# Kernel tuning notes

Measured on AMD Instinct MI355X. Metric: run time of the kernel, lower is better.

Reference implementation:

```python
import jax, jax.numpy as jnp
import numpy as np

SEQ_LEN = 1024
BATCH = 1024
TAG = 32
START = TAG - 2  # '[CLS]'
END = TAG - 1    # '[SEP]'
NEG = -10000.0


def setup_inputs() -> dict:
    key = jax.random.key(0)
    k1, k2, k3 = jax.random.split(key, 3)
    feats = jax.random.normal(k1, (SEQ_LEN, BATCH, TAG), dtype=jnp.float32)
    # valid-length mask: 1.0 for t < length, else 0.0 (float, as torch multiplies by it)
    lengths = jax.random.randint(k2, (BATCH,), SEQ_LEN // 2, SEQ_LEN + 1)
    mask = (jnp.arange(SEQ_LEN)[:, None] < lengths[None, :]).astype(jnp.float32)
    # transition parameter with forbidden moves into START and out of END
    transition = jax.random.normal(k3, (TAG, TAG), dtype=jnp.float32)
    transition = transition.at[START, :].set(NEG).at[:, END].set(NEG)
    return {"feats": feats, "mask": mask, "transition": transition}


def reference(feats, mask, transition):
    # feats: (S, B, T), mask: (S, B), transition: (T, T)
    batch, tag = feats.shape[1], feats.shape[2]
    alpha0 = jnp.full((batch, tag), NEG, dtype=feats.dtype).at[:, START].set(0.0)

    def step(alpha, xs):
        feat_t, mask_t = xs  # (B, T), (B,)
        # score[b, next, prev] = alpha[b, prev] + transition[next, prev] + feat_t[b, next]
        score = alpha[:, None, :] + transition[None, :, :] + feat_t[:, :, None]
        new_alpha = jax.nn.logsumexp(score, axis=-1)  # (B, T)
        m = mask_t[:, None]
        return new_alpha * m + alpha * (1.0 - m), None

    alpha, _ = jax.lax.scan(step, alpha0, (feats, mask))
    alpha = alpha + transition[END][None, :]
    return jax.nn.logsumexp(alpha, axis=-1)  # (B,)
```

## Files before the change

kernel.cpp:

```cpp
#include <hip/hip_runtime.h>

#define SEQ   1024
#define BATCH 1024
#define TAG   32
#define START 30
#define ENDT  31
#define PFD   8
#define HALF  512

__device__ __forceinline__ float rdlane(float v, int j) {
    return __uint_as_float(__builtin_amdgcn_readlane(__float_as_uint(v), j));
}

__device__ __forceinline__ void gather_dot(float v, const float* __restrict__ coef,
                                           float post, float& vn, float& lg) {
    float r[32];
    #pragma unroll
    for (int j = 0; j < 32; ++j) r[j] = rdlane(v, j);
    __builtin_amdgcn_sched_barrier(0);

    float s0 = r[0] * coef[0];
    float s1 = r[1] * coef[1];
    float s2 = r[2] * coef[2];
    float s3 = r[3] * coef[3];
    float s4 = r[4] * coef[4];
    float s5 = r[5] * coef[5];
    float s6 = r[6] * coef[6];
    float s7 = r[7] * coef[7];
    #pragma unroll
    for (int j = 1; j < 4; ++j) {
        s0 = fmaf(r[8 * j + 0], coef[8 * j + 0], s0);
        s1 = fmaf(r[8 * j + 1], coef[8 * j + 1], s1);
        s2 = fmaf(r[8 * j + 2], coef[8 * j + 2], s2);
        s3 = fmaf(r[8 * j + 3], coef[8 * j + 3], s3);
        s4 = fmaf(r[8 * j + 4], coef[8 * j + 4], s4);
        s5 = fmaf(r[8 * j + 5], coef[8 * j + 5], s5);
        s6 = fmaf(r[8 * j + 6], coef[8 * j + 6], s6);
        s7 = fmaf(r[8 * j + 7], coef[8 * j + 7], s7);
    }
    float dot = ((s0 + s1) + (s2 + s3)) + ((s4 + s5) + (s6 + s7));

    float c  = fmaxf(r[0], 1e-20f);
    float rr = __builtin_amdgcn_rcpf(c);
    lg = __logf(c);
    float sc = post * rr;
    vn = dot * sc;
}

__device__ __forceinline__ void crf_core(float v, float fval,
                                         const float* __restrict__ e,
                                         float& vn, float& lg) {
    gather_dot(v, e, __expf(fval), vn, lg);
}

__device__ void slow_path(const float* __restrict__ feats,
                          const float* __restrict__ mask,
                          const float* __restrict__ trans,
                          float* __restrict__ out, int b, int lane) {
    const int i = lane & 31;
    float e[32];
    {
        const float4* tr4 = reinterpret_cast<const float4*>(trans + i * TAG);
        #pragma unroll
        for (int c = 0; c < 8; ++c) {
            float4 t = tr4[c];
            e[4 * c + 0] = __expf(t.x);
            e[4 * c + 1] = __expf(t.y);
            e[4 * c + 2] = __expf(t.z);
            e[4 * c + 3] = __expf(t.w);
        }
    }
    const float* fp = feats + (unsigned)(b * TAG + i);
    const float* mk = mask + (unsigned)b;

    float  v  = (i == START) ? 1.0f : 0.0f;
    double mA = 0.0;

    float fb[PFD], mb[PFD];
    #pragma unroll
    for (int p = 0; p < PFD; ++p) {
        fb[p] = fp[(unsigned)p << 15];
        mb[p] = mk[(unsigned)p << 10];
    }
    for (int t = 0; t < SEQ; t += PFD) {
        #pragma unroll
        for (int p = 0; p < PFD; ++p) {
            unsigned mu = __builtin_amdgcn_readfirstlane(__float_as_uint(mb[p]));
            float fv = fb[p];
            int tn = t + PFD + p; tn = (tn < SEQ) ? tn : (SEQ - 1);
            fb[p] = fp[(unsigned)tn << 15];
            mb[p] = mk[(unsigned)tn << 10];
            if (mu != 0u) {
                float vn, lg;
                crf_core(v, fv, e, vn, lg);
                if (mu == 0x3f800000u) {
                    v = vn;
                    mA += (double)lg;
                } else {
                    float m   = __uint_as_float(mu);
                    float lv  = __logf(fmaxf(v,  1e-37f));
                    float lvn = __logf(fmaxf(vn, 1e-37f));
                    v = v * __expf(m * (lvn - lv));
                    mA += (double)(m * lg);
                }
            }
        }
    }
    float z = v * __expf(trans[ENDT * TAG + i]);
    float mx = z;
    #pragma unroll
    for (int k = 16; k >= 1; k >>= 1)
        mx = fmaxf(mx, __shfl_xor(mx, k, 32));
    float ss = z * __builtin_amdgcn_rcpf(mx);
    #pragma unroll
    for (int k = 16; k >= 1; k >>= 1)
        ss += __shfl_xor(ss, k, 32);
    if (lane == 0)
        out[b] = (float)(mA + (double)__logf(mx) + (double)__logf(ss));
}

__global__ __launch_bounds__(128, 2) void crf_fwd_kernel(
    const float* __restrict__ feats,
    const float* __restrict__ mask,
    const float* __restrict__ trans,
    float* __restrict__ out)
{
    const int tid  = threadIdx.x;
    const int lane = tid & 63;
    const int w    = tid >> 6;
    const int i    = lane & 31;
    const int b    = blockIdx.x;

    __shared__ float  sX[32], sY[32];
    __shared__ double sM[2];
    __shared__ int    sFrac;

    if (tid == 0) sFrac = 0;
    __syncthreads();

    {
        const int tb = w * HALF;
        bool bad = false;
        #pragma unroll
        for (int k = 0; k < 8; ++k) {
            float m = mask[(unsigned)((tb + k * 64 + lane) * BATCH + b)];
            bad |= (m != 0.0f) & (m != 1.0f);
        }
        if (__ballot(bad)) sFrac = 1;
    }
    __syncthreads();

    if (sFrac) {
        if (w == 0) slow_path(feats, mask, trans, out, b, lane);
        return;
    }

    const float* fp = feats + (unsigned)(b * TAG + i);
    const float* mk = mask + (unsigned)b;

    if (w == 0) {
        float e[32];
        const float4* tr4 = reinterpret_cast<const float4*>(trans + i * TAG);
        #pragma unroll
        for (int c = 0; c < 8; ++c) {
            float4 t = tr4[c];
            e[4 * c + 0] = __expf(t.x);
            e[4 * c + 1] = __expf(t.y);
            e[4 * c + 2] = __expf(t.z);
            e[4 * c + 3] = __expf(t.w);
        }
        float  v  = (i == START) ? 1.0f : 0.0f;
        double mA = 0.0;

        float fb[PFD], mb[PFD];
        #pragma unroll
        for (int p = 0; p < PFD; ++p) {
            fb[p] = fp[(unsigned)p << 15];
            mb[p] = mk[(unsigned)p << 10];
        }
        for (int t = 0; t < HALF; t += PFD) {
            #pragma unroll
            for (int p = 0; p < PFD; ++p) {
                unsigned mu = __builtin_amdgcn_readfirstlane(__float_as_uint(mb[p]));
                float fv = fb[p];
                int tn = t + PFD + p;
                fb[p] = fp[(unsigned)tn << 15];
                mb[p] = mk[(unsigned)tn << 10];
                if (mu != 0u) {
                    float vn, lg;
                    gather_dot(v, e, __expf(fv), vn, lg);
                    v = vn; mA += (double)lg;
                }
            }
        }
        if (lane < 32) sX[i] = v;
        if (lane == 0) sM[0] = mA;
    } else {
        float eT[32];
        #pragma unroll
        for (int c = 0; c < 32; ++c)
            eT[c] = __expf(trans[c * TAG + i]);
        float  y  = __expf(trans[ENDT * TAG + i]);
        double mB = 0.0;

        float fb[PFD], mb[PFD];
        #pragma unroll
        for (int p = 0; p < PFD; ++p) {
            fb[p] = fp[(unsigned)(SEQ - 1 - p) << 15];
            mb[p] = mk[(unsigned)(SEQ - 1 - p) << 10];
        }
        for (int s = 0; s < HALF; s += PFD) {
            #pragma unroll
            for (int p = 0; p < PFD; ++p) {
                unsigned mu = __builtin_amdgcn_readfirstlane(__float_as_uint(mb[p]));
                float fv = fb[p];
                int tn = SEQ - 1 - (s + PFD + p);
                fb[p] = fp[(unsigned)tn << 15];
                mb[p] = mk[(unsigned)tn << 10];
                if (mu != 0u) {
                    float u = y * __expf(fv);
                    float yn, lg;
                    gather_dot(u, eT, 1.0f, yn, lg);
                    y = yn; mB += (double)lg;
                }
            }
        }
        if (lane < 32) sY[i] = y;
        if (lane == 0) sM[1] = mB;
    }
    __syncthreads();

    if (w == 0) {
        float z = sX[i] * sY[i];
        float mx = z;
        #pragma unroll
        for (int k = 16; k >= 1; k >>= 1)
            mx = fmaxf(mx, __shfl_xor(mx, k, 32));
        mx = fmaxf(mx, 1e-30f);
        float ss = z * __builtin_amdgcn_rcpf(mx);
        #pragma unroll
        for (int k = 16; k >= 1; k >>= 1)
            ss += __shfl_xor(ss, k, 32);
        if (lane == 0)
            out[b] = (float)(sM[0] + sM[1]
                             + (double)__logf(mx) + (double)__logf(ss));
    }
}

extern "C" void kernel_launch(void* const* d_in, const int* in_sizes, int n_in,
                              void* d_out, int out_size, void* d_ws, size_t ws_size,
                              hipStream_t stream) {
    const float* feats = (const float*)d_in[0];
    const float* mask  = (const float*)d_in[1];
    const float* trans = (const float*)d_in[2];
    float* out = (float*)d_out;
    crf_fwd_kernel<<<dim3(BATCH), dim3(128), 0, stream>>>(feats, mask, trans, out);
}
```

Baseline: 319.5 us.

## Split each CRF recurrence dot product across both wave halves using ds_bpermute

The fast path now splits each 32-term dot product across the two 32-lane halves of the wavefront. Each half gathers 16 alpha values with ds_bpermute and multiplies them by its half of the exp(transition) row. The halves then combine their partial sums with a cross-half shuffle. This replaces 32 serial readlane (scalar) reads per step with 16 LDS-crossbar permutes and halves the FMA chain, aiming to shorten the per-timestep critical path, at the cost of extra permute latency and one more shuffle.

Result: slower. 355.9 us (+11.4%).

```diff
diff --git a/kernel.cpp b/kernel.cpp
--- a/kernel.cpp
+++ b/kernel.cpp
@@ -11,9 +11,12 @@
 __device__ __forceinline__ float rdlane(float v, int j) {
     return __uint_as_float(__builtin_amdgcn_readlane(__float_as_uint(v), j));
 }
-
-__device__ __forceinline__ void gather_dot(float v, const float* __restrict__ coef,
-                                           float post, float& vn, float& lg) {
+__device__ __forceinline__ float rdfirst(float v) {
+    return __uint_as_float(__builtin_amdgcn_readfirstlane(__float_as_uint(v)));
+}
+
+__device__ __forceinline__ void gather_dot_full(float v, const float* __restrict__ coef,
+                                                float post, float& vn, float& lg) {
     float r[32];
     #pragma unroll
     for (int j = 0; j < 32; ++j) r[j] = rdlane(v, j);
@@ -47,10 +50,38 @@
     vn = dot * sc;
 }
 
-__device__ __forceinline__ void crf_core(float v, float fval,
-                                         const float* __restrict__ e,
-                                         float& vn, float& lg) {
-    gather_dot(v, e, __expf(fval), vn, lg);
+__device__ __forceinline__ void step16(float v, const float* __restrict__ eh,
+                                       float post, int vbase, float& vn, float& lg) {
+    float r[16];
+    #pragma unroll
+    for (int j = 0; j < 16; ++j)
+        r[j] = __uint_as_float((unsigned)__builtin_amdgcn_ds_bpermute(
+                   vbase + 4 * j, (int)__float_as_uint(v)));
+
+    float c  = fmaxf(rdfirst(v), 1e-20f);
+    float rr = __builtin_amdgcn_rcpf(c);
+    lg = __logf(c);
+    float sc = post * rr;
+
+    float s0 = r[0] * eh[0];
+    float s1 = r[1] * eh[1];
+    float s2 = r[2] * eh[2];
+    float s3 = r[3] * eh[3];
+    float s4 = r[4] * eh[4];
+    float s5 = r[5] * eh[5];
+    float s6 = r[6] * eh[6];
+    float s7 = r[7] * eh[7];
+    s0 = fmaf(r[8],  eh[8],  s0);
+    s1 = fmaf(r[9],  eh[9],  s1);
+    s2 = fmaf(r[10], eh[10], s2);
+    s3 = fmaf(r[11], eh[11], s3);
+    s4 = fmaf(r[12], eh[12], s4);
+    s5 = fmaf(r[13], eh[13], s5);
+    s6 = fmaf(r[14], eh[14], s6);
+    s7 = fmaf(r[15], eh[15], s7);
+    float d = ((s0 + s1) + (s2 + s3)) + ((s4 + s5) + (s6 + s7));
+    d += __shfl_xor(d, 32);
+    vn = d * sc;
 }
 
 __device__ void slow_path(const float* __restrict__ feats,
@@ -92,7 +123,7 @@
             mb[p] = mk[(unsigned)tn << 10];
             if (mu != 0u) {
                 float vn, lg;
-                crf_core(v, fv, e, vn, lg);
+                gather_dot_full(v, e, __expf(fv), vn, lg);
                 if (mu == 0x3f800000u) {
                     v = vn;
                     mA += (double)lg;
@@ -129,7 +160,9 @@
     const int lane = tid & 63;
     const int w    = tid >> 6;
     const int i    = lane & 31;
+    const int h    = lane >> 5;
     const int b    = blockIdx.x;
+    const int vbase = (lane & 32) * 6;
 
     __shared__ float  sX[32], sY[32];
     __shared__ double sM[2];
@@ -159,16 +192,11 @@
     const float* mk = mask + (unsigned)b;
 
     if (w == 0) {
-        float e[32];
-        const float4* tr4 = reinterpret_cast<const float4*>(trans + i * TAG);
-        #pragma unroll
-        for (int c = 0; c < 8; ++c) {
-            float4 t = tr4[c];
-            e[4 * c + 0] = __expf(t.x);
-            e[4 * c + 1] = __expf(t.y);
-            e[4 * c + 2] = __expf(t.z);
-            e[4 * c + 3] = __expf(t.w);
-        }
+        float eh[16];
+        #pragma unroll
+        for (int j = 0; j < 16; ++j)
+            eh[j] = __expf(trans[i * TAG + 16 * h + j]);
+
         float  v  = (i == START) ? 1.0f : 0.0f;
         double mA = 0.0;
 
@@ -188,7 +216,7 @@
                 mb[p] = mk[(unsigned)tn << 10];
                 if (mu != 0u) {
                     float vn, lg;
-                    gather_dot(v, e, __expf(fv), vn, lg);
+                    step16(v, eh, __expf(fv), vbase, vn, lg);
                     v = vn; mA += (double)lg;
                 }
             }
@@ -196,10 +224,11 @@
         if (lane < 32) sX[i] = v;
         if (lane == 0) sM[0] = mA;
     } else {
-        float eT[32];
-        #pragma unroll
-        for (int c = 0; c < 32; ++c)
-            eT[c] = __expf(trans[c * TAG + i]);
+        float ehT[16];
+        #pragma unroll
+        for (int j = 0; j < 16; ++j)
+            ehT[j] = __expf(trans[(16 * h + j) * TAG + i]);
+
         float  y  = __expf(trans[ENDT * TAG + i]);
         double mB = 0.0;
 
@@ -220,7 +249,7 @@
                 if (mu != 0u) {
                     float u = y * __expf(fv);
                     float yn, lg;
-                    gather_dot(u, eT, 1.0f, yn, lg);
+                    step16(u, ehT, 1.0f, vbase, yn, lg);
                     y = yn; mB += (double)lg;
                 }
             }
```
